# Performance work log

Measured on AMD Instinct MI355X. Metric: run time of the kernel, lower is better.

The kernel has to match this reference:

```python
import jax, jax.numpy as jnp
import numpy as np

B, S, D, H, DH, RANK = 1, 2048, 1024, 16, 64, 16
NUM_ITERS = 5
EPS = 1e-6


def setup_inputs() -> dict:
    ks = jax.random.split(jax.random.key(0), 8)
    scale = 1.0 / np.sqrt(D)
    return {
        "x": jax.random.normal(ks[0], (B, S, D), dtype=jnp.float32),
        "Wq": jax.random.normal(ks[1], (D, D), dtype=jnp.float32) * scale,
        "Wk": jax.random.normal(ks[2], (D, D), dtype=jnp.float32) * scale,
        "Wv": jax.random.normal(ks[3], (D, D), dtype=jnp.float32) * scale,
        "Wo": jax.random.normal(ks[4], (D, D), dtype=jnp.float32) * scale,
        "bandwidth": jnp.array(1.0, dtype=jnp.float32),
        "diag_scale": jnp.ones((1, H, 1), dtype=jnp.float32),
        "pos_embedding": jax.random.normal(ks[5], (2048, RANK), dtype=jnp.float32) * 0.02,
        "head_proj": jax.random.normal(ks[6], (H, RANK, RANK), dtype=jnp.float32) * 0.02,
        "reg": jnp.array(0.1, dtype=jnp.float32),
        "lambda_reg": jnp.array(0.1, dtype=jnp.float32),
    }


def reference(x, Wq, Wk, Wv, Wo, bandwidth, diag_scale, pos_embedding, head_proj, reg, lambda_reg):
    b, s, d = x.shape
    h, dh = H, DH

    def heads(t):  # (b,s,d) -> (b,h,s,dh)
        return t.reshape(b, s, h, dh).transpose(0, 2, 1, 3)

    q = heads(x @ Wq)
    k = heads(x @ Wk)
    v = heads(x @ Wv)

    # RBF kernel via norm trick: ||q-k||^2 = ||q||^2 + ||k||^2 - 2 q.k
    bw = jax.nn.softplus(bandwidth) + EPS
    q_nsq = jnp.sum(q * q, axis=-1, keepdims=True)            # (b,h,s,1)
    k_nsq = jnp.sum(k * k, axis=-1, keepdims=True)            # (b,h,s,1)
    dist_sq = q_nsq + jnp.swapaxes(k_nsq, -2, -1) - 2.0 * jnp.einsum('bhsd,bhtd->bhst', q, k)
    dist_sq = jnp.maximum(dist_sq, 0.0)
    K = jnp.exp(-dist_sq / (2.0 * bw * bw))                   # (b,h,s,s)

    lam = jax.nn.softplus(lambda_reg)

    # Preconditioner P = diag(d) + U U^T
    kdiag = jnp.diagonal(K, axis1=-2, axis2=-1)               # (b,h,s)
    diag_p = jax.nn.softplus(kdiag) * diag_scale + reg        # (b,h,s)
    U = jnp.einsum('sr,hrp->hsp', pos_embedding[:s], head_proj)  # (h,s,rank)

    # Preconditioned Richardson iteration for (K + lam I) alpha = V
    alpha = jnp.zeros_like(v)
    for _ in range(NUM_ITERS):
        r = v - (jnp.einsum('bhst,bhtd->bhsd', K, alpha) + lam * alpha)
        ut_r = jnp.einsum('htr,bhtd->bhrd', U, r)
        p = r * diag_p[..., None] + jnp.einsum('hsr,bhrd->bhsd', U, ut_r)
        alpha = alpha + p

    out = jnp.einsum('bhst,bhtd->bhsd', K, alpha)             # output = K alpha
    out = out.transpose(0, 2, 1, 3).reshape(b, s, d) @ Wo
    return out
```

## Files before the change

### kernel.cpp

```cpp
#include <hip/hip_runtime.h>
#include <cstdint>
#include <cstddef>

constexpr int kS  = 2048;
constexpr int kD  = 1024;
constexpr int kH  = 16;
constexpr int kDH = 64;
constexpr int kR  = 16;

typedef __attribute__((ext_vector_type(8))) short bf16x8;
typedef __attribute__((ext_vector_type(4))) float f32x4;

__device__ __forceinline__ unsigned short kar_f2bf(float x) {
  unsigned u = __float_as_uint(x);
  return (unsigned short)((u + 0x7FFFu + ((u >> 16) & 1u)) >> 16);
}
__device__ __forceinline__ float kar_bf2f(short h) {
  return __uint_as_float((unsigned)(unsigned short)h << 16);
}
__device__ __forceinline__ void kar_split_bf(float x, short& hi, short& lo) {
  unsigned short h = kar_f2bf(x);
  float hf = __uint_as_float((unsigned)h << 16);
  hi = (short)h;
  lo = (short)kar_f2bf(x - hf);
}

__global__ __launch_bounds__(64) void kar_scalars_kernel(const float* __restrict__ bw,
                                                         const float* __restrict__ lreg,
                                                         double* __restrict__ SC) {
  if (threadIdx.x == 0) {
    double b = log1p(exp((double)bw[0])) + 1e-6;
    SC[0] = 1.0 / (2.0 * b * b);
    SC[1] = log1p(exp((double)lreg[0]));
  }
}

__global__ __launch_bounds__(256) void kar_u_kernel(const float* __restrict__ pe,
                                                    const float* __restrict__ hp,
                                                    float* __restrict__ U) {
  int o = blockIdx.x * 256 + threadIdx.x;
  int r = o & 15, s = (o >> 4) & 2047, h = o >> 15;
  double acc = 0.0;
#pragma unroll
  for (int rp = 0; rp < kR; rp++)
    acc += (double)pe[s * kR + rp] * (double)hp[((h * kR) + rp) * kR + r];
  U[o] = (float)acc;
}

__global__ __launch_bounds__(256) void kar_utr_partial_kernel(
    const float* __restrict__ Ubuf, const float* __restrict__ rbuf,
    double* __restrict__ utrp) {
  const int h  = blockIdx.y;
  const int sb = blockIdx.x * 64;
  const int t  = threadIdx.x;
  __shared__ float Uch[32][16];
  __shared__ float Rch[32][64];
  double acc[4] = {};
  for (int cs = 0; cs < 64; cs += 32) {
    __syncthreads();
    if (t < 128) {
      const int i = t >> 2, f = (t & 3) * 4;
      *(float4*)&Uch[i][f] = *(const float4*)&Ubuf[((size_t)(h * kS) + sb + cs + i) * kR + f];
    }
#pragma unroll
    for (int rep = 0; rep < 2; rep++) {
      const int e = t + rep * 256;
      const int i = e >> 4, c = (e & 15) * 4;
      *(float4*)&Rch[i][c] = *(const float4*)&rbuf[((size_t)(h * kS) + sb + cs + i) * kDH + c];
    }
    __syncthreads();
    for (int i = 0; i < 32; i++) {
#pragma unroll
      for (int rep = 0; rep < 4; rep++) {
        const int p = t + rep * 256;
        const int r = p >> 6, d = p & 63;
        acc[rep] += (double)Uch[i][r] * (double)Rch[i][d];
      }
    }
  }
#pragma unroll
  for (int rep = 0; rep < 4; rep++) {
    const int p = t + rep * 256;
    const int r = p >> 6, d = p & 63;
    utrp[(((size_t)(h * 32) + blockIdx.x) * kR + r) * kDH + d] = acc[rep];
  }
}

__global__ __launch_bounds__(256) void kar_utr_reduce_kernel(const double* __restrict__ utrp,
                                                             double* __restrict__ utr) {
  int o = blockIdx.x * 256 + threadIdx.x;
  int h = o >> 10, rd = o & 1023;
  double s = 0.0;
#pragma unroll
  for (int j = 0; j < 32; j++) s += utrp[(size_t)h * 32768 + (size_t)j * 1024 + rd];
  utr[o] = s;
}

__global__ __launch_bounds__(256) void kar_update_kernel(
    const float* __restrict__ rsrc, const double* __restrict__ dgp,
    const float* __restrict__ Ubuf, const double* __restrict__ utr,
    float* __restrict__ alpha, int first) {
  int e = blockIdx.x * 256 + threadIdx.x;
  const int d = e & 63;
  const int s = (e >> 6) & 2047;
  const int h = e >> 17;
  const double rv = (double)rsrc[e];
  const double dp = dgp[h * kS + s];
  const float*  Us = &Ubuf[((size_t)(h * kS) + s) * kR];
  const double* uh = &utr[(size_t)h * kR * kDH];
  double sum = 0.0;
#pragma unroll
  for (int ri = 0; ri < kR; ri++) sum += (double)Us[ri] * uh[ri * kDH + d];
  const double p = rv * dp + sum;
  const double an = (first ? 0.0 : (double)alpha[e]) + p;
  alpha[e] = (float)an;
}

__global__ __launch_bounds__(256) void kar_update_t_kernel(
    const float* __restrict__ rsrc, const double* __restrict__ dgp,
    const float* __restrict__ Ubuf, const double* __restrict__ utr,
    float* __restrict__ alpha, short* __restrict__ ath, int first) {
  const int h = blockIdx.y, s0 = blockIdx.x * 64;
  __shared__ float T[64][65];
  const int t = threadIdx.x;
  const int r16 = t >> 4, c4 = (t & 15) * 4;
  const double* uh = &utr[(size_t)h * kR * kDH];
#pragma unroll
  for (int it = 0; it < 4; it++) {
    const int row = it * 16 + r16;
    const int s = s0 + row;
    const size_t eg = ((size_t)h * kS + s) * kDH + c4;
    const float4 rv4 = *(const float4*)&rsrc[eg];
    const double dp = dgp[h * kS + s];
    const float* Us = &Ubuf[((size_t)h * kS + s) * kR];
    double sum0 = 0.0, sum1 = 0.0, sum2 = 0.0, sum3 = 0.0;
#pragma unroll
    for (int ri = 0; ri < kR; ri++) {
      const double u = (double)Us[ri];
      const double* ur = &uh[ri * kDH + c4];
      sum0 += u * ur[0]; sum1 += u * ur[1];
      sum2 += u * ur[2]; sum3 += u * ur[3];
    }
    double a0 = (first ? 0.0 : (double)alpha[eg + 0]) + ((double)rv4.x * dp + sum0);
    double a1 = (first ? 0.0 : (double)alpha[eg + 1]) + ((double)rv4.y * dp + sum1);
    double a2 = (first ? 0.0 : (double)alpha[eg + 2]) + ((double)rv4.z * dp + sum2);
    double a3 = (first ? 0.0 : (double)alpha[eg + 3]) + ((double)rv4.w * dp + sum3);
    float4 o;
    o.x = (float)a0; o.y = (float)a1; o.z = (float)a2; o.w = (float)a3;
    *(float4*)&alpha[eg] = o;
    T[row][c4] = o.x; T[row][c4 + 1] = o.y; T[row][c4 + 2] = o.z; T[row][c4 + 3] = o.w;
  }
  __syncthreads();
#pragma unroll
  for (int it = 0; it < 4; it++) {
    int d = it * 16 + r16;
    float v0 = T[c4][d], v1 = T[c4 + 1][d], v2 = T[c4 + 2][d], v3 = T[c4 + 3][d];
    *(short4*)&ath[((size_t)h * kDH + d) * kS + s0 + c4] =
        make_short4((short)kar_f2bf(v0), (short)kar_f2bf(v1),
                    (short)kar_f2bf(v2), (short)kar_f2bf(v3));
  }
}


__global__ __launch_bounds__(256) void kar_xsplit_kernel(const float* __restrict__ x,
                                                         short* __restrict__ xh,
                                                         short* __restrict__ xl) {
  size_t e = ((size_t)blockIdx.x * 256 + threadIdx.x) * 4;
  float4 a = *(const float4*)&x[e];
  short h0, l0, h1, l1, h2, l2, h3, l3;
  kar_split_bf(a.x, h0, l0); kar_split_bf(a.y, h1, l1);
  kar_split_bf(a.z, h2, l2); kar_split_bf(a.w, h3, l3);
  *(short4*)&xh[e] = make_short4(h0, h1, h2, h3);
  *(short4*)&xl[e] = make_short4(l0, l1, l2, l3);
}

__global__ __launch_bounds__(256) void kar_wsplit_kernel(
    const float* __restrict__ Wq, const float* __restrict__ Wk,
    const float* __restrict__ Wv, const float* __restrict__ Wo,
    short* __restrict__ WTh, short* __restrict__ WTl) {
  const float* W = (blockIdx.z == 0) ? Wq : (blockIdx.z == 1) ? Wk
                 : (blockIdx.z == 2) ? Wv : Wo;
  short* oh = WTh + (size_t)blockIdx.z * kD * kD;
  short* ol = WTl + (size_t)blockIdx.z * kD * kD;
  const int n0 = blockIdx.x * 64, k0 = blockIdx.y * 64;
  __shared__ float T[64][65];
  const int t = threadIdx.x;
  const int r16 = t >> 4, c4 = (t & 15) * 4;
#pragma unroll
  for (int it = 0; it < 4; it++) {
    int r = it * 16 + r16;
    float4 a = *(const float4*)&W[(size_t)(k0 + r) * kD + n0 + c4];
    T[r][c4] = a.x; T[r][c4 + 1] = a.y; T[r][c4 + 2] = a.z; T[r][c4 + 3] = a.w;
  }
  __syncthreads();
#pragma unroll
  for (int it = 0; it < 4; it++) {
    int n = it * 16 + r16;
    float v0 = T[c4][n], v1 = T[c4 + 1][n], v2 = T[c4 + 2][n], v3 = T[c4 + 3][n];
    short h0, l0, h1, l1, h2, l2, h3, l3;
    kar_split_bf(v0, h0, l0); kar_split_bf(v1, h1, l1);
    kar_split_bf(v2, h2, l2); kar_split_bf(v3, h3, l3);
    *(short4*)&oh[(size_t)(n0 + n) * kD + k0 + c4] = make_short4(h0, h1, h2, h3);
    *(short4*)&ol[(size_t)(n0 + n) * kD + k0 + c4] = make_short4(l0, l1, l2, l3);
  }
}

__global__ __launch_bounds__(256) void kar_mfma_gemm_qkv_kernel(
    const short* __restrict__ xh, const short* __restrict__ xl,
    const short* __restrict__ WTh, const short* __restrict__ WTl,
    float* __restrict__ v,
    short* __restrict__ qsh, short* __restrict__ qsl,
    short* __restrict__ ksh, short* __restrict__ ksl) {
  const int z = blockIdx.z;
  const short* Bh = WTh + (size_t)z * kD * kD;
  const short* Bl = WTl + (size_t)z * kD * kD;
  const int n0 = blockIdx.x * 64;
  const int m0 = blockIdx.y * 128;
  constexpr int LW = 40;
  __shared__ short Xh[128 * LW], Xl[128 * LW], Wh[64 * LW], Wl[64 * LW];
  const int t = threadIdx.x, lane = t & 63, wv = t >> 6;
  const int wm = wv >> 1, wn = wv & 1, l16 = lane & 15, qd = lane >> 4;
  f32x4 acc[4][2];
#pragma unroll
  for (int i = 0; i < 4; i++)
#pragma unroll
    for (int j = 0; j < 2; j++) acc[i][j] = (f32x4){0.f, 0.f, 0.f, 0.f};
  const int xrow = t >> 1, xc = (t & 1) * 16;
  for (int k0 = 0; k0 < kD; k0 += 32) {
    __syncthreads();
    {
      const size_t xs = (size_t)(m0 + xrow) * kD + k0 + xc;
      *(bf16x8*)&Xh[xrow * LW + xc]     = *(const bf16x8*)&xh[xs];
      *(bf16x8*)&Xh[xrow * LW + xc + 8] = *(const bf16x8*)&xh[xs + 8];
      *(bf16x8*)&Xl[xrow * LW + xc]     = *(const bf16x8*)&xl[xs];
      *(bf16x8*)&Xl[xrow * LW + xc + 8] = *(const bf16x8*)&xl[xs + 8];
    }
    if (t < 128) {
      const int wrow = t >> 1, wc = (t & 1) * 16;
      const size_t wsrc = (size_t)(n0 + wrow) * kD + k0 + wc;
      *(bf16x8*)&Wh[wrow * LW + wc]     = *(const bf16x8*)&Bh[wsrc];
      *(bf16x8*)&Wh[wrow * LW + wc + 8] = *(const bf16x8*)&Bh[wsrc + 8];
    } else {
      const int t2 = t - 128, wrow = t2 >> 1, wc = (t2 & 1) * 16;
      const size_t wsrc = (size_t)(n0 + wrow) * kD + k0 + wc;
      *(bf16x8*)&Wl[wrow * LW + wc]     = *(const bf16x8*)&Bl[wsrc];
      *(bf16x8*)&Wl[wrow * LW + wc + 8] = *(const bf16x8*)&Bl[wsrc + 8];
    }
    __syncthreads();
    bf16x8 bH[2], bL[2];
#pragma unroll
    for (int ni = 0; ni < 2; ni++) {
      const int rn = wn * 32 + ni * 16 + l16;
      bH[ni] = *(const bf16x8*)&Wh[rn * LW + qd * 8];
      bL[ni] = *(const bf16x8*)&Wl[rn * LW + qd * 8];
    }
#pragma unroll
    for (int mi = 0; mi < 4; mi++) {
      const int rm = wm * 64 + mi * 16 + l16;
      const bf16x8 aH = *(const bf16x8*)&Xh[rm * LW + qd * 8];
      const bf16x8 aL = *(const bf16x8*)&Xl[rm * LW + qd * 8];
#pragma unroll
      for (int ni = 0; ni < 2; ni++) {
        acc[mi][ni] = __builtin_amdgcn_mfma_f32_16x16x32_bf16(aH, bH[ni], acc[mi][ni], 0, 0, 0);
        acc[mi][ni] = __builtin_amdgcn_mfma_f32_16x16x32_bf16(aL, bH[ni], acc[mi][ni], 0, 0, 0);
        acc[mi][ni] = __builtin_amdgcn_mfma_f32_16x16x32_bf16(aH, bL[ni], acc[mi][ni], 0, 0, 0);
      }
    }
  }
  const int h = blockIdx.x;
#pragma unroll
  for (int mi = 0; mi < 4; mi++)
#pragma unroll
    for (int ni = 0; ni < 2; ni++) {
      const int d = wn * 32 + ni * 16 + l16;
#pragma unroll
      for (int r = 0; r < 4; r++) {
        const int s = m0 + wm * 64 + mi * 16 + qd * 4 + r;
        const float val = acc[mi][ni][r];
        const size_t idx = (((size_t)h * kS) + s) * kDH + d;
        if (z == 2) {
          v[idx] = val;
        } else {
          short hh, ll; kar_split_bf(val, hh, ll);
          if (z == 0) { qsh[idx] = hh; qsl[idx] = ll; }
          else        { ksh[idx] = hh; ksl[idx] = ll; }
        }
      }
    }
}

__global__ __launch_bounds__(256) void kar_mfma_gemm_wo_kernel(
    const short* __restrict__ th, const short* __restrict__ tl,
    const short* __restrict__ Bh, const short* __restrict__ Bl,
    float* __restrict__ outp) {
  const int n0 = blockIdx.x * 64;
  const int m0 = blockIdx.y * 128;
  constexpr int LW = 40;
  __shared__ short Xh[128 * LW], Xl[128 * LW], Wh[64 * LW], Wl[64 * LW];
  const int t = threadIdx.x, lane = t & 63, wv = t >> 6;
  const int wm = wv >> 1, wn = wv & 1, l16 = lane & 15, qd = lane >> 4;
  f32x4 acc[4][2];
#pragma unroll
  for (int i = 0; i < 4; i++)
#pragma unroll
    for (int j = 0; j < 2; j++) acc[i][j] = (f32x4){0.f, 0.f, 0.f, 0.f};
  const int xrow = t >> 1, xc = (t & 1) * 16;
  for (int k0 = 0; k0 < kD; k0 += 32) {
    __syncthreads();
    {
      const size_t xs = (size_t)(m0 + xrow) * kD + k0 + xc;
      *(bf16x8*)&Xh[xrow * LW + xc]     = *(const bf16x8*)&th[xs];
      *(bf16x8*)&Xh[xrow * LW + xc + 8] = *(const bf16x8*)&th[xs + 8];
      *(bf16x8*)&Xl[xrow * LW + xc]     = *(const bf16x8*)&tl[xs];
      *(bf16x8*)&Xl[xrow * LW + xc + 8] = *(const bf16x8*)&tl[xs + 8];
    }
    if (t < 128) {
      const int wrow = t >> 1, wc = (t & 1) * 16;
      const size_t wsrc = (size_t)(n0 + wrow) * kD + k0 + wc;
      *(bf16x8*)&Wh[wrow * LW + wc]     = *(const bf16x8*)&Bh[wsrc];
      *(bf16x8*)&Wh[wrow * LW + wc + 8] = *(const bf16x8*)&Bh[wsrc + 8];
    } else {
      const int t2 = t - 128, wrow = t2 >> 1, wc = (t2 & 1) * 16;
      const size_t wsrc = (size_t)(n0 + wrow) * kD + k0 + wc;
      *(bf16x8*)&Wl[wrow * LW + wc]     = *(const bf16x8*)&Bl[wsrc];
      *(bf16x8*)&Wl[wrow * LW + wc + 8] = *(const bf16x8*)&Bl[wsrc + 8];
    }
    __syncthreads();
    bf16x8 bH[2], bL[2];
#pragma unroll
    for (int ni = 0; ni < 2; ni++) {
      const int rn = wn * 32 + ni * 16 + l16;
      bH[ni] = *(const bf16x8*)&Wh[rn * LW + qd * 8];
      bL[ni] = *(const bf16x8*)&Wl[rn * LW + qd * 8];
    }
#pragma unroll
    for (int mi = 0; mi < 4; mi++) {
      const int rm = wm * 64 + mi * 16 + l16;
      const bf16x8 aH = *(const bf16x8*)&Xh[rm * LW + qd * 8];
      const bf16x8 aL = *(const bf16x8*)&Xl[rm * LW + qd * 8];
#pragma unroll
      for (int ni = 0; ni < 2; ni++) {
        acc[mi][ni] = __builtin_amdgcn_mfma_f32_16x16x32_bf16(aH, bH[ni], acc[mi][ni], 0, 0, 0);
        acc[mi][ni] = __builtin_amdgcn_mfma_f32_16x16x32_bf16(aL, bH[ni], acc[mi][ni], 0, 0, 0);
        acc[mi][ni] = __builtin_amdgcn_mfma_f32_16x16x32_bf16(aH, bL[ni], acc[mi][ni], 0, 0, 0);
      }
    }
  }
#pragma unroll
  for (int mi = 0; mi < 4; mi++)
#pragma unroll
    for (int ni = 0; ni < 2; ni++) {
      const int col = n0 + wn * 32 + ni * 16 + l16;
#pragma unroll
      for (int r = 0; r < 4; r++) {
        const int s = m0 + wm * 64 + mi * 16 + qd * 4 + r;
        outp[(size_t)s * kD + col] = acc[mi][ni][r];
      }
    }
}

__global__ __launch_bounds__(256) void kar_norms2_kernel(
    const short* __restrict__ qsh, const short* __restrict__ qsl,
    const short* __restrict__ ksh, const short* __restrict__ ksl,
    double* __restrict__ qn, double* __restrict__ kn) {
  int o = blockIdx.x * 256 + threadIdx.x;
  const short *sh, *sl; double* dst; int p;
  if (o < kH * kS) { sh = qsh; sl = qsl; dst = qn; p = o; }
  else             { sh = ksh; sl = ksl; dst = kn; p = o - kH * kS; }
  const short* rh = sh + (size_t)p * kDH;
  const short* rl = sl + (size_t)p * kDH;
  double s = 0.0;
  for (int i = 0; i < kDH; i += 4) {
    short4 a = *(const short4*)&rh[i];
    short4 b = *(const short4*)&rl[i];
    double e0 = (double)kar_bf2f(a.x) + (double)kar_bf2f(b.x);
    double e1 = (double)kar_bf2f(a.y) + (double)kar_bf2f(b.y);
    double e2 = (double)kar_bf2f(a.z) + (double)kar_bf2f(b.z);
    double e3 = (double)kar_bf2f(a.w) + (double)kar_bf2f(b.w);
    s += e0 * e0 + e1 * e1 + e2 * e2 + e3 * e3;
  }
  dst[p] = s;
}

__global__ __launch_bounds__(256) void kar_diagp2_kernel(
    const short* __restrict__ qsh, const short* __restrict__ qsl,
    const short* __restrict__ ksh, const short* __restrict__ ksl,
    const double* __restrict__ qn, const double* __restrict__ kn,
    const double* __restrict__ SC, const float* __restrict__ dsc,
    const float* __restrict__ reg, double* __restrict__ dgp) {
  int o = blockIdx.x * 256 + threadIdx.x;
  int h = o >> 11;
  const short* qh = qsh + (size_t)o * kDH;
  const short* ql = qsl + (size_t)o * kDH;
  const short* kh = ksh + (size_t)o * kDH;
  const short* kl = ksl + (size_t)o * kDH;
  double dot = 0.0;
  for (int i = 0; i < kDH; i++) {
    double qi = (double)kar_bf2f(qh[i]) + (double)kar_bf2f(ql[i]);
    double ki = (double)kar_bf2f(kh[i]) + (double)kar_bf2f(kl[i]);
    dot += qi * ki;
  }
  double dist = fmax(qn[o] + kn[o] - 2.0 * dot, 0.0);
  double Kss = exp(-dist * SC[0]);
  double sp  = log1p(exp(Kss));
  dgp[o] = sp * (double)dsc[h] + (double)reg[0];
}

template <bool FINAL>
__global__ __launch_bounds__(256, 2) void kar_mfma_iter5_kernel(
    const short* __restrict__ qsh, const short* __restrict__ qsl,
    const short* __restrict__ ksh, const short* __restrict__ ksl,
    const short* __restrict__ ath,
    const float* __restrict__ alpha, const float* __restrict__ v,
    const double* __restrict__ qn, const double* __restrict__ kn,
    const double* __restrict__ SC, float* __restrict__ outp,
    short* __restrict__ tmph, short* __restrict__ tmpl,
    const float* __restrict__ Ug, double* __restrict__ utrp) {
  constexpr int LDW = 72;
  __shared__ short Kh[64 * LDW], Kl[64 * LDW];
  __shared__ short Ah[64 * LDW];
  __shared__ short Ph[64 * LDW];
  __shared__ float qns[64];
  __shared__ float Ub[64][16];
  const int h   = blockIdx.y;
  const int s0  = blockIdx.x * 64;
  const int tid = threadIdx.x;
  const int lane = tid & 63;
  const int wv   = tid >> 6;
  const int l16  = lane & 15;
  const int qd   = lane >> 4;
  const int row = tid >> 2, c8 = (tid & 3) * 16;
  bf16x8 qH[4][2], qL[4][2];
#pragma unroll
  for (int sq = 0; sq < 4; sq++) {
    const size_t qb = (((size_t)h * kS) + s0 + sq * 16 + l16) * kDH;
    qH[sq][0] = *(const bf16x8*)&qsh[qb + qd * 8];
    qH[sq][1] = *(const bf16x8*)&qsh[qb + 32 + qd * 8];
    qL[sq][0] = *(const bf16x8*)&qsl[qb + qd * 8];
    qL[sq][1] = *(const bf16x8*)&qsl[qb + 32 + qd * 8];
  }
  if (tid < 64) qns[tid] = (float)qn[h * kS + s0 + tid];
  const float cc = (float)SC[0];
  f32x4 acco[4];
#pragma unroll
  for (int i = 0; i < 4; i++) acco[i] = (f32x4){0.f, 0.f, 0.f, 0.f};

  for (int t0 = 0; t0 < kS; t0 += 64) {
    __syncthreads();
    {
      const size_t ksrc = (((size_t)h * kS) + t0 + row) * kDH;
      *(bf16x8*)&Kh[row * LDW + c8]     = *(const bf16x8*)&ksh[ksrc + c8];
      *(bf16x8*)&Kh[row * LDW + c8 + 8] = *(const bf16x8*)&ksh[ksrc + c8 + 8];
      *(bf16x8*)&Kl[row * LDW + c8]     = *(const bf16x8*)&ksl[ksrc + c8];
      *(bf16x8*)&Kl[row * LDW + c8 + 8] = *(const bf16x8*)&ksl[ksrc + c8 + 8];
      const size_t asrc = ((size_t)h * kDH + row) * kS + t0;
      *(bf16x8*)&Ah[row * LDW + c8]     = *(const bf16x8*)&ath[asrc + c8];
      *(bf16x8*)&Ah[row * LDW + c8 + 8] = *(const bf16x8*)&ath[asrc + c8 + 8];
    }
    const float knr = (float)kn[h * kS + t0 + wv * 16 + l16];
    __syncthreads();
    f32x4 accp[4];
#pragma unroll
    for (int i = 0; i < 4; i++) accp[i] = (f32x4){0.f, 0.f, 0.f, 0.f};
#pragma unroll
    for (int kt = 0; kt < 2; kt++) {
      const int ko = kt * 32 + qd * 8;
      const bf16x8 bH = *(const bf16x8*)&Kh[(wv * 16 + l16) * LDW + ko];
      const bf16x8 bL = *(const bf16x8*)&Kl[(wv * 16 + l16) * LDW + ko];
#pragma unroll
      for (int sq = 0; sq < 4; sq++) {
        accp[sq] = __builtin_amdgcn_mfma_f32_16x16x32_bf16(qH[sq][kt], bH, accp[sq], 0, 0, 0);
        accp[sq] = __builtin_amdgcn_mfma_f32_16x16x32_bf16(qL[sq][kt], bH, accp[sq], 0, 0, 0);
        accp[sq] = __builtin_amdgcn_mfma_f32_16x16x32_bf16(qH[sq][kt], bL, accp[sq], 0, 0, 0);
      }
    }
#pragma unroll
    for (int sq = 0; sq < 4; sq++) {
#pragma unroll
      for (int r = 0; r < 4; r++) {
        const int srow = sq * 16 + qd * 4 + r;
        const float e2 = fmaf(2.0f, accp[sq][r], -(qns[srow] + knr));
        const float val = __expf(fminf(e2, 0.0f) * cc);
        Ph[srow * LDW + wv * 16 + l16] = (short)kar_f2bf(val);
      }
    }
    __syncthreads();
#pragma unroll
    for (int kt = 0; kt < 2; kt++) {
      const int ko = kt * 32 + qd * 8;
      const bf16x8 bH = *(const bf16x8*)&Ah[(wv * 16 + l16) * LDW + ko];
#pragma unroll
      for (int sq = 0; sq < 4; sq++) {
        const bf16x8 pH = *(const bf16x8*)&Ph[(sq * 16 + l16) * LDW + ko];
        acco[sq] = __builtin_amdgcn_mfma_f32_16x16x32_bf16(pH, bH, acco[sq], 0, 0, 0);
      }
    }
  }
  const int d = wv * 16 + l16;
  if (FINAL) {
#pragma unroll
    for (int sq = 0; sq < 4; sq++) {
#pragma unroll
      for (int r = 0; r < 4; r++) {
        const int s = s0 + sq * 16 + qd * 4 + r;
        short hh, ll; kar_split_bf(acco[sq][r], hh, ll);
        tmph[(size_t)s * kD + h * kDH + d] = hh;
        tmpl[(size_t)s * kD + h * kDH + d] = ll;
      }
    }
  } else {
    const float lamf = (float)SC[1];
    float rv[4][4];
#pragma unroll
    for (int sq = 0; sq < 4; sq++) {
#pragma unroll
      for (int r = 0; r < 4; r++) {
        const int s = s0 + sq * 16 + qd * 4 + r;
        const size_t eg = ((size_t)h * kS + s) * kDH + d;
        const float rr = v[eg] - (acco[sq][r] + lamf * alpha[eg]);
        rv[sq][r] = rr;
        outp[eg] = rr;
      }
    }
    *(float4*)&Ub[tid >> 2][(tid & 3) * 4] =
        *(const float4*)&Ug[((size_t)h * kS + s0 + (tid >> 2)) * kR + (tid & 3) * 4];
    __syncthreads();
    double uacc[16];
#pragma unroll
    for (int ri = 0; ri < 16; ri++) uacc[ri] = 0.0;
#pragma unroll
    for (int sq = 0; sq < 4; sq++) {
#pragma unroll
      for (int r = 0; r < 4; r++) {
        const int sl = sq * 16 + qd * 4 + r;
        const double rval = (double)rv[sq][r];
        const float4 u0 = *(const float4*)&Ub[sl][0];
        const float4 u1 = *(const float4*)&Ub[sl][4];
        const float4 u2 = *(const float4*)&Ub[sl][8];
        const float4 u3 = *(const float4*)&Ub[sl][12];
        uacc[0]  += (double)u0.x * rval; uacc[1]  += (double)u0.y * rval;
        uacc[2]  += (double)u0.z * rval; uacc[3]  += (double)u0.w * rval;
        uacc[4]  += (double)u1.x * rval; uacc[5]  += (double)u1.y * rval;
        uacc[6]  += (double)u1.z * rval; uacc[7]  += (double)u1.w * rval;
        uacc[8]  += (double)u2.x * rval; uacc[9]  += (double)u2.y * rval;
        uacc[10] += (double)u2.z * rval; uacc[11] += (double)u2.w * rval;
        uacc[12] += (double)u3.x * rval; uacc[13] += (double)u3.y * rval;
        uacc[14] += (double)u3.z * rval; uacc[15] += (double)u3.w * rval;
      }
    }
#pragma unroll
    for (int ri = 0; ri < 16; ri++) {
      uacc[ri] += __shfl_xor(uacc[ri], 16, 64);
      uacc[ri] += __shfl_xor(uacc[ri], 32, 64);
    }
    if (qd == 0) {
#pragma unroll
      for (int ri = 0; ri < 16; ri++)
        utrp[(((size_t)(h * 32) + blockIdx.x) * kR + ri) * kDH + d] = uacc[ri];
    }
  }
}

__global__ __launch_bounds__(256) void kar_gemm_qkv_f32_kernel(
    const float* __restrict__ x,
    const float* __restrict__ Wq, const float* __restrict__ Wk, const float* __restrict__ Wv,
    float* __restrict__ q, float* __restrict__ k, float* __restrict__ v) {
  const float* W = (blockIdx.z == 0) ? Wq : (blockIdx.z == 1) ? Wk : Wv;
  float* outp    = (blockIdx.z == 0) ? q  : (blockIdx.z == 1) ? k  : v;
  const int n0 = blockIdx.x * 64;
  const int m0 = blockIdx.y * 64;
  const int tid = threadIdx.x;
  const int tx = tid & 15, ty = tid >> 4;
  __shared__ float As[16][68];
  __shared__ float Bs[16][68];
  double acc[4][4] = {};
  const int lr = tid >> 2;
  const int lk = (tid & 3) * 4;
  const int br = tid >> 4;
  const int bc = (tid & 15) * 4;
  for (int k0 = 0; k0 < kD; k0 += 16) {
    const float4 a4 = *(const float4*)&x[(size_t)(m0 + lr) * kD + k0 + lk];
    const float4 b4 = *(const float4*)&W[(size_t)(k0 + br) * kD + n0 + bc];
    __syncthreads();
    As[lk + 0][lr] = a4.x; As[lk + 1][lr] = a4.y;
    As[lk + 2][lr] = a4.z; As[lk + 3][lr] = a4.w;
    *(float4*)&Bs[br][bc] = b4;
    __syncthreads();
    float c32[4][4] = {};
#pragma unroll
    for (int kk = 0; kk < 16; kk++) {
      const float4 av = *(const float4*)&As[kk][ty * 4];
      const float4 bv = *(const float4*)&Bs[kk][tx * 4];
      const float a_[4] = {av.x, av.y, av.z, av.w};
      const float b_[4] = {bv.x, bv.y, bv.z, bv.w};
#pragma unroll
      for (int i = 0; i < 4; i++)
#pragma unroll
        for (int j = 0; j < 4; j++) c32[i][j] = fmaf(a_[i], b_[j], c32[i][j]);
    }
#pragma unroll
    for (int i = 0; i < 4; i++)
#pragma unroll
      for (int j = 0; j < 4; j++) acc[i][j] += (double)c32[i][j];
  }
  const int h = n0 >> 6;
#pragma unroll
  for (int i = 0; i < 4; i++) {
    const int s = m0 + ty * 4 + i;
    float4 o;
    o.x = (float)acc[i][0]; o.y = (float)acc[i][1];
    o.z = (float)acc[i][2]; o.w = (float)acc[i][3];
    *(float4*)&outp[((size_t)h * kS + s) * kDH + tx * 4] = o;
  }
}

__global__ __launch_bounds__(256) void kar_gemm_plain_kernel(
    const float* __restrict__ A, const float* __restrict__ W, float* __restrict__ C) {
  const int n0 = blockIdx.x * 64;
  const int m0 = blockIdx.y * 64;
  const int tid = threadIdx.x;
  const int tx = tid & 15, ty = tid >> 4;
  __shared__ float As[16][68];
  __shared__ float Bs[16][68];
  double acc[4][4] = {};
  const int lr = tid >> 2;
  const int lk = (tid & 3) * 4;
  const int br = tid >> 4;
  const int bc = (tid & 15) * 4;
  for (int k0 = 0; k0 < kD; k0 += 16) {
    const float4 a4 = *(const float4*)&A[(size_t)(m0 + lr) * kD + k0 + lk];
    const float4 b4 = *(const float4*)&W[(size_t)(k0 + br) * kD + n0 + bc];
    __syncthreads();
    As[lk + 0][lr] = a4.x; As[lk + 1][lr] = a4.y;
    As[lk + 2][lr] = a4.z; As[lk + 3][lr] = a4.w;
    *(float4*)&Bs[br][bc] = b4;
    __syncthreads();
    float c32[4][4] = {};
#pragma unroll
    for (int kk = 0; kk < 16; kk++) {
      const float4 av = *(const float4*)&As[kk][ty * 4];
      const float4 bv = *(const float4*)&Bs[kk][tx * 4];
      const float a_[4] = {av.x, av.y, av.z, av.w};
      const float b_[4] = {bv.x, bv.y, bv.z, bv.w};
#pragma unroll
      for (int i = 0; i < 4; i++)
#pragma unroll
        for (int j = 0; j < 4; j++) c32[i][j] = fmaf(a_[i], b_[j], c32[i][j]);
    }
#pragma unroll
    for (int i = 0; i < 4; i++)
#pragma unroll
      for (int j = 0; j < 4; j++) acc[i][j] += (double)c32[i][j];
  }
#pragma unroll
  for (int i = 0; i < 4; i++) {
    const int s = m0 + ty * 4 + i;
    float4 o;
    o.x = (float)acc[i][0]; o.y = (float)acc[i][1];
    o.z = (float)acc[i][2]; o.w = (float)acc[i][3];
    *(float4*)&C[(size_t)s * kD + n0 + tx * 4] = o;
  }
}

__global__ __launch_bounds__(256) void kar_norms_f32_kernel(const float* __restrict__ q,
                                                            const float* __restrict__ k,
                                                            double* __restrict__ qn,
                                                            double* __restrict__ kn) {
  int o = blockIdx.x * 256 + threadIdx.x;
  const float* src; double* dst; int p;
  if (o < kH * kS) { src = q; dst = qn; p = o; }
  else             { src = k; dst = kn; p = o - kH * kS; }
  const float* rowp = src + (size_t)p * kDH;
  double s = 0.0;
  for (int i = 0; i < kDH; i += 4) {
    float4 x4 = *(const float4*)&rowp[i];
    s += (double)x4.x * (double)x4.x + (double)x4.y * (double)x4.y +
         (double)x4.z * (double)x4.z + (double)x4.w * (double)x4.w;
  }
  dst[p] = s;
}

__global__ __launch_bounds__(256) void kar_diagp_f32_kernel(
    const float* __restrict__ q, const float* __restrict__ k,
    const double* __restrict__ qn, const double* __restrict__ kn,
    const double* __restrict__ SC, const float* __restrict__ dsc,
    const float* __restrict__ reg, double* __restrict__ dgp) {
  int o = blockIdx.x * 256 + threadIdx.x;
  int h = o >> 11;
  const float* qp = q + (size_t)o * kDH;
  const float* kp = k + (size_t)o * kDH;
  double dot = 0.0;
  for (int i = 0; i < kDH; i++) dot += (double)qp[i] * (double)kp[i];
  double dist = fmax(qn[o] + kn[o] - 2.0 * dot, 0.0);
  double Kss = exp(-dist * SC[0]);
  double sp  = log1p(exp(Kss));
  dgp[o] = sp * (double)dsc[h] + (double)reg[0];
}

template <bool FINAL>
__global__ __launch_bounds__(256, 2) void kar_mfma_iterA_kernel(
    const float* __restrict__ q, const float* __restrict__ k,
    const float* __restrict__ alpha, const float* __restrict__ v,
    const double* __restrict__ qn, const double* __restrict__ kn,
    const double* __restrict__ SC, float* __restrict__ outp) {
  constexpr int LDW = 72;
  __shared__ short Qh[64 * LDW], Ql[64 * LDW];
  __shared__ short Kh[64 * LDW], Kl[64 * LDW];
  __shared__ short Ph[64 * LDW], Pl[64 * LDW];
  __shared__ short Ah[64 * LDW], Al[64 * LDW];
  __shared__ float qns[64], kns[64];
  const int h   = blockIdx.y;
  const int s0  = blockIdx.x * 64;
  const int tid = threadIdx.x;
  const int lane = tid & 63;
  const int wv   = tid >> 6;
  const int l16  = lane & 15;
  const int qd   = lane >> 4;
  const int m16  = wv * 16;
  const float* qh = q + ((size_t)h * kS + s0) * kDH;
  const float* kh = k + (size_t)h * kS * kDH;
  const float* ah = alpha + (size_t)h * kS * kDH;
  {
    const int row = tid >> 4;
    const int c4  = (tid & 15) * 4;
#pragma unroll
    for (int rep = 0; rep < 4; rep++) {
      const int r = rep * 16 + row;
      const float4 a = *(const float4*)&qh[(size_t)r * kDH + c4];
      short h0, l0, h1, l1, h2, l2, h3, l3;
      kar_split_bf(a.x, h0, l0); kar_split_bf(a.y, h1, l1);
      kar_split_bf(a.z, h2, l2); kar_split_bf(a.w, h3, l3);
      *(short4*)&Qh[r * LDW + c4] = make_short4(h0, h1, h2, h3);
      *(short4*)&Ql[r * LDW + c4] = make_short4(l0, l1, l2, l3);
    }
    if (tid < 64) qns[tid] = (float)qn[h * kS + s0 + tid];
  }
  const float cc = (float)SC[0];
  f32x4 acco[4];
#pragma unroll
  for (int i = 0; i < 4; i++) acco[i] = (f32x4){0.f, 0.f, 0.f, 0.f};
  for (int t0 = 0; t0 < kS; t0 += 64) {
    __syncthreads();
    {
      const int row = tid >> 4;
      const int c4  = (tid & 15) * 4;
#pragma unroll
      for (int rep = 0; rep < 4; rep++) {
        const int r = rep * 16 + row;
        const float4 b = *(const float4*)&kh[(size_t)(t0 + r) * kDH + c4];
        short h0, l0, h1, l1, h2, l2, h3, l3;
        kar_split_bf(b.x, h0, l0); kar_split_bf(b.y, h1, l1);
        kar_split_bf(b.z, h2, l2); kar_split_bf(b.w, h3, l3);
        *(short4*)&Kh[r * LDW + c4] = make_short4(h0, h1, h2, h3);
        *(short4*)&Kl[r * LDW + c4] = make_short4(l0, l1, l2, l3);
        const float4 av = *(const float4*)&ah[(size_t)(t0 + r) * kDH + c4];
        kar_split_bf(av.x, h0, l0); kar_split_bf(av.y, h1, l1);
        kar_split_bf(av.z, h2, l2); kar_split_bf(av.w, h3, l3);
        Ah[(c4 + 0) * LDW + r] = h0; Al[(c4 + 0) * LDW + r] = l0;
        Ah[(c4 + 1) * LDW + r] = h1; Al[(c4 + 1) * LDW + r] = l1;
        Ah[(c4 + 2) * LDW + r] = h2; Al[(c4 + 2) * LDW + r] = l2;
        Ah[(c4 + 3) * LDW + r] = h3; Al[(c4 + 3) * LDW + r] = l3;
      }
      if (tid < 64) kns[tid] = (float)kn[h * kS + t0 + tid];
    }
    __syncthreads();
    f32x4 accp[4];
#pragma unroll
    for (int i = 0; i < 4; i++) accp[i] = (f32x4){0.f, 0.f, 0.f, 0.f};
#pragma unroll
    for (int kt = 0; kt < 2; kt++) {
      const int ko = kt * 32 + qd * 8;
      const bf16x8 aH = *(const bf16x8*)&Qh[(m16 + l16) * LDW + ko];
      const bf16x8 aL = *(const bf16x8*)&Ql[(m16 + l16) * LDW + ko];
#pragma unroll
      for (int nt = 0; nt < 4; nt++) {
        const bf16x8 bH = *(const bf16x8*)&Kh[(nt * 16 + l16) * LDW + ko];
        const bf16x8 bL = *(const bf16x8*)&Kl[(nt * 16 + l16) * LDW + ko];
        accp[nt] = __builtin_amdgcn_mfma_f32_16x16x32_bf16(aH, bH, accp[nt], 0, 0, 0);
        accp[nt] = __builtin_amdgcn_mfma_f32_16x16x32_bf16(aL, bH, accp[nt], 0, 0, 0);
        accp[nt] = __builtin_amdgcn_mfma_f32_16x16x32_bf16(aH, bL, accp[nt], 0, 0, 0);
      }
    }
#pragma unroll
    for (int nt = 0; nt < 4; nt++) {
      const int tcol = nt * 16 + l16;
      const float kv = kns[tcol];
#pragma unroll
      for (int r = 0; r < 4; r++) {
        const int srow = m16 + qd * 4 + r;
        const float e2 = fmaf(2.0f, accp[nt][r], -(qns[srow] + kv));
        const float val = __expf(fminf(e2, 0.0f) * cc);
        short hb, lb; kar_split_bf(val, hb, lb);
        Ph[srow * LDW + tcol] = hb;
        Pl[srow * LDW + tcol] = lb;
      }
    }
#pragma unroll
    for (int kt = 0; kt < 2; kt++) {
      const int ko = kt * 32 + qd * 8;
      const bf16x8 pH = *(const bf16x8*)&Ph[(m16 + l16) * LDW + ko];
      const bf16x8 pL = *(const bf16x8*)&Pl[(m16 + l16) * LDW + ko];
#pragma unroll
      for (int dt = 0; dt < 4; dt++) {
        const bf16x8 bH = *(const bf16x8*)&Ah[(dt * 16 + l16) * LDW + ko];
        const bf16x8 bL = *(const bf16x8*)&Al[(dt * 16 + l16) * LDW + ko];
        acco[dt] = __builtin_amdgcn_mfma_f32_16x16x32_bf16(pH, bH, acco[dt], 0, 0, 0);
        acco[dt] = __builtin_amdgcn_mfma_f32_16x16x32_bf16(pL, bH, acco[dt], 0, 0, 0);
        acco[dt] = __builtin_amdgcn_mfma_f32_16x16x32_bf16(pH, bL, acco[dt], 0, 0, 0);
      }
    }
  }
  if (FINAL) {
#pragma unroll
    for (int dt = 0; dt < 4; dt++) {
#pragma unroll
      for (int r = 0; r < 4; r++) {
        const int s = s0 + m16 + qd * 4 + r;
        const int d = dt * 16 + l16;
        outp[(size_t)s * kD + h * kDH + d] = acco[dt][r];
      }
    }
  } else {
    const float lamf = (float)SC[1];
#pragma unroll
    for (int dt = 0; dt < 4; dt++) {
#pragma unroll
      for (int r = 0; r < 4; r++) {
        const int s = s0 + m16 + qd * 4 + r;
        const int d = dt * 16 + l16;
        const size_t eg = ((size_t)h * kS + s) * kDH + d;
        outp[eg] = v[eg] - (acco[dt][r] + lamf * alpha[eg]);
      }
    }
  }
}

extern "C" void kernel_launch(void* const* d_in, const int* in_sizes, int n_in,
                              void* d_out, int out_size, void* d_ws, size_t ws_size,
                              hipStream_t stream) {
  (void)in_sizes; (void)n_in; (void)out_size;
  const float* x    = (const float*)d_in[0];
  const float* Wq   = (const float*)d_in[1];
  const float* Wk   = (const float*)d_in[2];
  const float* Wv   = (const float*)d_in[3];
  const float* Wo   = (const float*)d_in[4];
  const float* bw   = (const float*)d_in[5];
  const float* dsc  = (const float*)d_in[6];
  const float* pe   = (const float*)d_in[7];
  const float* hp   = (const float*)d_in[8];
  const float* reg  = (const float*)d_in[9];
  const float* lreg = (const float*)d_in[10];
  float* out = (float*)d_out;

  char* w = (char*)d_ws;
  size_t off = 0;
  auto take = [&](size_t bytes) -> void* {
    void* p = w + off;
    off += (bytes + 255) & ~(size_t)255;
    return p;
  };
  const size_t HSD = (size_t)kH * kS * kDH;

  float*  v_    = (float*)take(HSD * 4);
  float*  alpha = (float*)take(HSD * 4);
  float*  rbuf  = (float*)take(HSD * 4);
  short*  qsh   = (short*)take(HSD * 2);
  short*  qsl   = (short*)take(HSD * 2);
  short*  ksh   = (short*)take(HSD * 2);
  short*  ksl   = (short*)take(HSD * 2);
  short*  ath   = (short*)take(HSD * 2);
  short*  xh    = (short*)take((size_t)kS * kD * 2);
  short*  xl    = (short*)take((size_t)kS * kD * 2);
  short*  WTh   = (short*)take((size_t)4 * kD * kD * 2);
  short*  WTl   = (short*)take((size_t)4 * kD * kD * 2);
  double* qn    = (double*)take((size_t)kH * kS * 8);
  double* kn    = (double*)take((size_t)kH * kS * 8);
  double* dgp   = (double*)take((size_t)kH * kS * 8);
  float*  U     = (float*)take((size_t)kH * kS * kR * 4);
  double* utr   = (double*)take((size_t)kH * kR * kDH * 8);
  double* utrp  = (double*)take((size_t)kH * 32 * kR * kDH * 8);
  double* SC    = (double*)take(256);
  const size_t need_new = off;

  if (ws_size >= need_new) {
    kar_scalars_kernel<<<1, 64, 0, stream>>>(bw, lreg, SC);
    kar_xsplit_kernel<<<2048, 256, 0, stream>>>(x, xh, xl);
    kar_wsplit_kernel<<<dim3(16, 16, 4), 256, 0, stream>>>(Wq, Wk, Wv, Wo, WTh, WTl);
    kar_mfma_gemm_qkv_kernel<<<dim3(16, 16, 3), 256, 0, stream>>>(
        xh, xl, WTh, WTl, v_, qsh, qsl, ksh, ksl);
    kar_norms2_kernel<<<256, 256, 0, stream>>>(qsh, qsl, ksh, ksl, qn, kn);
    kar_u_kernel<<<2048, 256, 0, stream>>>(pe, hp, U);
    kar_diagp2_kernel<<<128, 256, 0, stream>>>(qsh, qsl, ksh, ksl, qn, kn, SC, dsc, reg, dgp);

    kar_utr_partial_kernel<<<dim3(32, kH), 256, 0, stream>>>(U, v_, utrp);
    kar_utr_reduce_kernel<<<64, 256, 0, stream>>>(utrp, utr);
    kar_update_t_kernel<<<dim3(32, kH), 256, 0, stream>>>(v_, dgp, U, utr, alpha, ath, 1);

    for (int it = 1; it < 5; it++) {
      kar_mfma_iter5_kernel<false><<<dim3(32, kH), 256, 0, stream>>>(
          qsh, qsl, ksh, ksl, ath, alpha, v_, qn, kn, SC, rbuf, nullptr, nullptr, U, utrp);
      kar_utr_reduce_kernel<<<64, 256, 0, stream>>>(utrp, utr);
      kar_update_t_kernel<<<dim3(32, kH), 256, 0, stream>>>(rbuf, dgp, U, utr, alpha, ath, 0);
    }

    kar_mfma_iter5_kernel<true><<<dim3(32, kH), 256, 0, stream>>>(
        qsh, qsl, ksh, ksl, ath, alpha, v_, qn, kn, SC, rbuf, xh, xl, U, utrp);
    kar_mfma_gemm_wo_kernel<<<dim3(16, 16), 256, 0, stream>>>(
        xh, xl, WTh + (size_t)3 * kD * kD, WTl + (size_t)3 * kD * kD, out);
  } else {
    size_t off2 = 0;
    auto take2 = [&](size_t bytes) -> void* {
      void* p = w + off2;
      off2 += (bytes + 255) & ~(size_t)255;
      return p;
    };
    float*  q2    = (float*)take2(HSD * 4);
    float*  k2    = (float*)take2(HSD * 4);
    float*  v2    = (float*)take2(HSD * 4);
    float*  al2   = (float*)take2(HSD * 4);
    float*  rb2   = (float*)take2(HSD * 4);
    float*  tmp2  = (float*)take2((size_t)kS * kD * 4);
    double* qn2   = (double*)take2((size_t)kH * kS * 8);
    double* kn2   = (double*)take2((size_t)kH * kS * 8);
    double* dgp2  = (double*)take2((size_t)kH * kS * 8);
    float*  U2    = (float*)take2((size_t)kH * kS * kR * 4);
    double* utr2  = (double*)take2((size_t)kH * kR * kDH * 8);
    double* utrp2 = (double*)take2((size_t)kH * 32 * kR * kDH * 8);
    double* SC2   = (double*)take2(256);

    kar_scalars_kernel<<<1, 64, 0, stream>>>(bw, lreg, SC2);
    kar_gemm_qkv_f32_kernel<<<dim3(16, 32, 3), 256, 0, stream>>>(x, Wq, Wk, Wv, q2, k2, v2);
    kar_norms_f32_kernel<<<256, 256, 0, stream>>>(q2, k2, qn2, kn2);
    kar_u_kernel<<<2048, 256, 0, stream>>>(pe, hp, U2);
    kar_diagp_f32_kernel<<<128, 256, 0, stream>>>(q2, k2, qn2, kn2, SC2, dsc, reg, dgp2);

    kar_utr_partial_kernel<<<dim3(32, kH), 256, 0, stream>>>(U2, v2, utrp2);
    kar_utr_reduce_kernel<<<64, 256, 0, stream>>>(utrp2, utr2);
    kar_update_kernel<<<8192, 256, 0, stream>>>(v2, dgp2, U2, utr2, al2, 1);

    for (int it = 1; it < 5; it++) {
      kar_mfma_iterA_kernel<false><<<dim3(32, kH), 256, 0, stream>>>(
          q2, k2, al2, v2, qn2, kn2, SC2, rb2);
      kar_utr_partial_kernel<<<dim3(32, kH), 256, 0, stream>>>(U2, rb2, utrp2);
      kar_utr_reduce_kernel<<<64, 256, 0, stream>>>(utrp2, utr2);
      kar_update_kernel<<<8192, 256, 0, stream>>>(rb2, dgp2, U2, utr2, al2, 0);
    }
    kar_mfma_iterA_kernel<true><<<dim3(32, kH), 256, 0, stream>>>(
        q2, k2, al2, v2, qn2, kn2, SC2, tmp2);
    kar_gemm_plain_kernel<<<dim3(16, 32), 256, 0, stream>>>(tmp2, Wo, out);
  }
}
```

Baseline: 612.6 us.

## Load K and alpha fragments directly from global, double-buffer P tile in LDS

The fused K-apply kernel no longer stages the K hi/lo and alpha^T tiles through shared memory. Each wave now reads its own MFMA B-operand fragments straight from global memory into registers. The P tile is double-buffered so one barrier per iteration replaces three, and the U tile load moves to the prologue. This cuts LDS traffic and synchronisation, but each K/alpha element is fetched by several waves through L1/L2 instead of once per block, and global latency is no longer hidden behind the LDS stage.

```diff
diff --git a/kernel.cpp b/kernel.cpp
--- a/kernel.cpp
+++ b/kernel.cpp
@@ -407,7 +407,7 @@
 }
 
 template <bool FINAL>
-__global__ __launch_bounds__(256, 2) void kar_mfma_iter5_kernel(
+__global__ __launch_bounds__(256, 2) void kar_mfma_iter6_kernel(
     const short* __restrict__ qsh, const short* __restrict__ qsl,
     const short* __restrict__ ksh, const short* __restrict__ ksl,
     const short* __restrict__ ath,
@@ -417,9 +417,7 @@
     short* __restrict__ tmph, short* __restrict__ tmpl,
     const float* __restrict__ Ug, double* __restrict__ utrp) {
   constexpr int LDW = 72;
-  __shared__ short Kh[64 * LDW], Kl[64 * LDW];
-  __shared__ short Ah[64 * LDW];
-  __shared__ short Ph[64 * LDW];
+  __shared__ short Ph[2][64 * LDW];
   __shared__ float qns[64];
   __shared__ float Ub[64][16];
   const int h   = blockIdx.y;
@@ -429,7 +427,6 @@
   const int wv   = tid >> 6;
   const int l16  = lane & 15;
   const int qd   = lane >> 4;
-  const int row = tid >> 2, c8 = (tid & 3) * 16;
   bf16x8 qH[4][2], qL[4][2];
 #pragma unroll
   for (int sq = 0; sq < 4; sq++) {
@@ -440,39 +437,44 @@
     qL[sq][1] = *(const bf16x8*)&qsl[qb + 32 + qd * 8];
   }
   if (tid < 64) qns[tid] = (float)qn[h * kS + s0 + tid];
+  if (!FINAL)
+    *(float4*)&Ub[tid >> 2][(tid & 3) * 4] =
+        *(const float4*)&Ug[((size_t)h * kS + s0 + (tid >> 2)) * kR + (tid & 3) * 4];
+  __syncthreads();
   const float cc = (float)SC[0];
   f32x4 acco[4];
 #pragma unroll
   for (int i = 0; i < 4; i++) acco[i] = (f32x4){0.f, 0.f, 0.f, 0.f};
 
-  for (int t0 = 0; t0 < kS; t0 += 64) {
-    __syncthreads();
-    {
-      const size_t ksrc = (((size_t)h * kS) + t0 + row) * kDH;
-      *(bf16x8*)&Kh[row * LDW + c8]     = *(const bf16x8*)&ksh[ksrc + c8];
-      *(bf16x8*)&Kh[row * LDW + c8 + 8] = *(const bf16x8*)&ksh[ksrc + c8 + 8];
-      *(bf16x8*)&Kl[row * LDW + c8]     = *(const bf16x8*)&ksl[ksrc + c8];
-      *(bf16x8*)&Kl[row * LDW + c8 + 8] = *(const bf16x8*)&ksl[ksrc + c8 + 8];
-      const size_t asrc = ((size_t)h * kDH + row) * kS + t0;
-      *(bf16x8*)&Ah[row * LDW + c8]     = *(const bf16x8*)&ath[asrc + c8];
-      *(bf16x8*)&Ah[row * LDW + c8 + 8] = *(const bf16x8*)&ath[asrc + c8 + 8];
-    }
-    const float knr = (float)kn[h * kS + t0 + wv * 16 + l16];
-    __syncthreads();
+  const short*  kRowH = &ksh[(((size_t)h * kS) + wv * 16 + l16) * kDH];
+  const short*  kRowL = &ksl[(((size_t)h * kS) + wv * 16 + l16) * kDH];
+  const short*  aRow  = &ath[((size_t)h * kDH + wv * 16 + l16) * kS];
+  const double* knp   = &kn[h * kS + wv * 16 + l16];
+
+  int buf = 0;
+  for (int t0 = 0; t0 < kS; t0 += 64, buf ^= 1) {
+    const size_t ko0 = (size_t)t0 * kDH + qd * 8;
+    const bf16x8 kH0 = *(const bf16x8*)&kRowH[ko0];
+    const bf16x8 kH1 = *(const bf16x8*)&kRowH[ko0 + 32];
+    const bf16x8 kL0 = *(const bf16x8*)&kRowL[ko0];
+    const bf16x8 kL1 = *(const bf16x8*)&kRowL[ko0 + 32];
+    const bf16x8 aH0 = *(const bf16x8*)&aRow[t0 + qd * 8];
+    const bf16x8 aH1 = *(const bf16x8*)&aRow[t0 + 32 + qd * 8];
+    const float  knr = (float)knp[t0];
     f32x4 accp[4];
 #pragma unroll
     for (int i = 0; i < 4; i++) accp[i] = (f32x4){0.f, 0.f, 0.f, 0.f};
 #pragma unroll
-    for (int kt = 0; kt < 2; kt++) {
-      const int ko = kt * 32 + qd * 8;
-      const bf16x8 bH = *(const bf16x8*)&Kh[(wv * 16 + l16) * LDW + ko];
-      const bf16x8 bL = *(const bf16x8*)&Kl[(wv * 16 + l16) * LDW + ko];
-#pragma unroll
-      for (int sq = 0; sq < 4; sq++) {
-        accp[sq] = __builtin_amdgcn_mfma_f32_16x16x32_bf16(qH[sq][kt], bH, accp[sq], 0, 0, 0);
-        accp[sq] = __builtin_amdgcn_mfma_f32_16x16x32_bf16(qL[sq][kt], bH, accp[sq], 0, 0, 0);
-        accp[sq] = __builtin_amdgcn_mfma_f32_16x16x32_bf16(qH[sq][kt], bL, accp[sq], 0, 0, 0);
-      }
+    for (int sq = 0; sq < 4; sq++) {
+      accp[sq] = __builtin_amdgcn_mfma_f32_16x16x32_bf16(qH[sq][0], kH0, accp[sq], 0, 0, 0);
+      accp[sq] = __builtin_amdgcn_mfma_f32_16x16x32_bf16(qL[sq][0], kH0, accp[sq], 0, 0, 0);
+      accp[sq] = __builtin_amdgcn_mfma_f32_16x16x32_bf16(qH[sq][0], kL0, accp[sq], 0, 0, 0);
+    }
+#pragma unroll
+    for (int sq = 0; sq < 4; sq++) {
+      accp[sq] = __builtin_amdgcn_mfma_f32_16x16x32_bf16(qH[sq][1], kH1, accp[sq], 0, 0, 0);
+      accp[sq] = __builtin_amdgcn_mfma_f32_16x16x32_bf16(qL[sq][1], kH1, accp[sq], 0, 0, 0);
+      accp[sq] = __builtin_amdgcn_mfma_f32_16x16x32_bf16(qH[sq][1], kL1, accp[sq], 0, 0, 0);
     }
 #pragma unroll
     for (int sq = 0; sq < 4; sq++) {
@@ -481,19 +483,16 @@
         const int srow = sq * 16 + qd * 4 + r;
         const float e2 = fmaf(2.0f, accp[sq][r], -(qns[srow] + knr));
         const float val = __expf(fminf(e2, 0.0f) * cc);
-        Ph[srow * LDW + wv * 16 + l16] = (short)kar_f2bf(val);
-      }
-    }
-    __syncthreads();
-#pragma unroll
-    for (int kt = 0; kt < 2; kt++) {
-      const int ko = kt * 32 + qd * 8;
-      const bf16x8 bH = *(const bf16x8*)&Ah[(wv * 16 + l16) * LDW + ko];
-#pragma unroll
-      for (int sq = 0; sq < 4; sq++) {
-        const bf16x8 pH = *(const bf16x8*)&Ph[(sq * 16 + l16) * LDW + ko];
-        acco[sq] = __builtin_amdgcn_mfma_f32_16x16x32_bf16(pH, bH, acco[sq], 0, 0, 0);
-      }
+        Ph[buf][srow * LDW + wv * 16 + l16] = (short)kar_f2bf(val);
+      }
+    }
+    __syncthreads();
+#pragma unroll
+    for (int sq = 0; sq < 4; sq++) {
+      const bf16x8 pH0 = *(const bf16x8*)&Ph[buf][(sq * 16 + l16) * LDW + qd * 8];
+      acco[sq] = __builtin_amdgcn_mfma_f32_16x16x32_bf16(pH0, aH0, acco[sq], 0, 0, 0);
+      const bf16x8 pH1 = *(const bf16x8*)&Ph[buf][(sq * 16 + l16) * LDW + 32 + qd * 8];
+      acco[sq] = __builtin_amdgcn_mfma_f32_16x16x32_bf16(pH1, aH1, acco[sq], 0, 0, 0);
     }
   }
   const int d = wv * 16 + l16;
@@ -522,9 +521,6 @@
         outp[eg] = rr;
       }
     }
-    *(float4*)&Ub[tid >> 2][(tid & 3) * 4] =
-        *(const float4*)&Ug[((size_t)h * kS + s0 + (tid >> 2)) * kR + (tid & 3) * 4];
-    __syncthreads();
     double uacc[16];
 #pragma unroll
     for (int ri = 0; ri < 16; ri++) uacc[ri] = 0.0;
@@ -897,13 +893,13 @@
     kar_update_t_kernel<<<dim3(32, kH), 256, 0, stream>>>(v_, dgp, U, utr, alpha, ath, 1);
 
     for (int it = 1; it < 5; it++) {
-      kar_mfma_iter5_kernel<false><<<dim3(32, kH), 256, 0, stream>>>(
+      kar_mfma_iter6_kernel<false><<<dim3(32, kH), 256, 0, stream>>>(
           qsh, qsl, ksh, ksl, ath, alpha, v_, qn, kn, SC, rbuf, nullptr, nullptr, U, utrp);
       kar_utr_reduce_kernel<<<64, 256, 0, stream>>>(utrp, utr);
       kar_update_t_kernel<<<dim3(32, kH), 256, 0, stream>>>(rbuf, dgp, U, utr, alpha, ath, 0);
     }
 
-    kar_mfma_iter5_kernel<true><<<dim3(32, kH), 256, 0, stream>>>(
+    kar_mfma_iter6_kernel<true><<<dim3(32, kH), 256, 0, stream>>>(
         qsh, qsl, ksh, ksl, ath, alpha, v_, qn, kn, SC, rbuf, xh, xl, U, utrp);
     kar_mfma_gemm_wo_kernel<<<dim3(16, 16), 256, 0, stream>>>(
         xh, xl, WTh + (size_t)3 * kD * kD, WTl + (size_t)3 * kD * kD, out);
```

Result: no change. 607.4 us (-0.8%).
